# Kernel tuning notes

Hardware: AMD Instinct MI355X
Metric: run time of the kernel (lower is better)

The kernel has to match this reference:

```python
import jax, jax.numpy as jnp
import numpy as np

EPS = 1e-5  # BatchNorm eps (torch default)


def point_sample(feat, points):
    """Bilinear sample feat [B,C,Hf,Wf] at points [B,K,2] (x,y in [0,1]),
    matching F.grid_sample(2*p-1, mode='bilinear', padding_mode='zeros',
    align_corners=False)."""
    B, C, Hf, Wf = feat.shape
    x = points[..., 0] * Wf - 0.5  # [B,K] pixel coords
    y = points[..., 1] * Hf - 0.5
    x0f = jnp.floor(x); y0f = jnp.floor(y)
    wx = (x - x0f)[:, None, :]  # [B,1,K]
    wy = (y - y0f)[:, None, :]
    x0 = x0f.astype(jnp.int32); y0 = y0f.astype(jnp.int32)
    flat = feat.reshape(B, C, Hf * Wf)

    def gather(xi, yi):
        valid = ((xi >= 0) & (xi < Wf) & (yi >= 0) & (yi < Hf))[:, None, :]
        lin = jnp.clip(yi, 0, Hf - 1) * Wf + jnp.clip(xi, 0, Wf - 1)  # [B,K]
        idx = jnp.broadcast_to(lin[:, None, :], (B, C, lin.shape[1]))
        return jnp.take_along_axis(flat, idx, axis=2) * valid

    v00 = gather(x0, y0)
    v10 = gather(x0 + 1, y0)
    v01 = gather(x0, y0 + 1)
    v11 = gather(x0 + 1, y0 + 1)
    return (v00 * (1 - wx) * (1 - wy) + v10 * wx * (1 - wy)
            + v01 * (1 - wx) * wy + v11 * wx * wy)


def bn(x, g, b, m, v):
    # eval-mode BatchNorm1d over channel dim of [B,C,K]
    scale = (g / jnp.sqrt(v + EPS))[None, :, None]
    return (x - m[None, :, None]) * scale + b[None, :, None]


def setup_inputs() -> dict:
    key = jax.random.key(0)
    ks = jax.random.split(key, 20)
    B, H, W = 8, 512, 512
    Cf = 256
    d = {
        'uncertainty_map': jax.random.normal(ks[0], (B, 1, H, W), jnp.float32),
        'prev_mask': jax.random.uniform(ks[1], (B, 1, H, W), jnp.float32),
        'enc_f': jax.random.normal(ks[2], (B, Cf, 128, 128), jnp.float32),
        'w1': jax.random.normal(ks[3], (256, Cf + 1), jnp.float32) * 0.05,
        'b1': jax.random.normal(ks[4], (256,), jnp.float32) * 0.05,
        'g1': jnp.ones((256,), jnp.float32),
        'be1': jnp.zeros((256,), jnp.float32),
        'm1': jax.random.normal(ks[5], (256,), jnp.float32) * 0.1,
        'v1': jax.random.uniform(ks[6], (256,), jnp.float32) + 0.5,
        'w2': jax.random.normal(ks[7], (256, 256), jnp.float32) * 0.05,
        'b2': jax.random.normal(ks[8], (256,), jnp.float32) * 0.05,
        'g2': jnp.ones((256,), jnp.float32),
        'be2': jnp.zeros((256,), jnp.float32),
        'm2': jax.random.normal(ks[9], (256,), jnp.float32) * 0.1,
        'v2': jax.random.uniform(ks[10], (256,), jnp.float32) + 0.5,
        'w3': jax.random.normal(ks[11], (1, 256), jnp.float32) * 0.05,
        'b3': jax.random.normal(ks[12], (1,), jnp.float32) * 0.05,
    }
    return d


def reference(uncertainty_map, prev_mask, enc_f,
              w1, b1, g1, be1, m1, v1,
              w2, b2, g2, be2, m2, v2,
              w3, b3):
    B, C, H, W = prev_mask.shape
    K = H * W // 10
    # K least-uncertain points (topk largest=False)
    _, idx = jax.lax.top_k(-uncertainty_map.reshape(B, -1), K)  # [B,K] int32
    col = (idx % W).astype(jnp.float32)
    row = (idx // W).astype(jnp.float32)
    points = jnp.stack([(col + 0.5) / W, (row + 0.5) / H], axis=-1)  # [B,K,2]

    coarse = point_sample(prev_mask, points)  # [B,1,K]
    fine = point_sample(enc_f, points)        # [B,Cf,K]
    h = jnp.concatenate([coarse, fine], axis=1)  # [B,Cf+1,K]

    h = jax.nn.relu(bn(jnp.einsum('oc,bck->bok', w1, h) + b1[None, :, None], g1, be1, m1, v1))
    h = jax.nn.relu(bn(jnp.einsum('oc,bck->bok', w2, h) + b2[None, :, None], g2, be2, m2, v2))
    refined = jax.nn.sigmoid(jnp.einsum('oc,bck->bok', w3, h) + b3[None, :, None])  # [B,1,K]

    flat = prev_mask.reshape(B, C, H * W)
    bi = jnp.arange(B)[:, None, None]
    ci = jnp.arange(C)[None, :, None]
    out = flat.at[bi, ci, idx[:, None, :]].set(jnp.broadcast_to(refined, (B, C, K)))
    return out.reshape(B, C, H, W)
```

## Files before the change

### kernel.cpp

```cpp
#include <hip/hip_runtime.h>
#include <hip/hip_bf16.h>

#define HW_IMG 262144
#define KSEL   26214
#define NB     8
#define CF     256
#define LDACT  264
#define GBLK   410
#define MBLK   205
#define NPTS_PAD 26240

#define ACOL(c) ((c) ^ ((((c) >> 6) & 3) << 4))

typedef short    short8 __attribute__((ext_vector_type(8)));
typedef float    f32x4  __attribute__((ext_vector_type(4)));
typedef unsigned u32x2  __attribute__((ext_vector_type(2)));
typedef unsigned short u16x4 __attribute__((ext_vector_type(4)));

__device__ __forceinline__ unsigned f2key(float f){
    unsigned u = __builtin_bit_cast(unsigned, f);
    return (u & 0x80000000u) ? ~u : (u | 0x80000000u);
}
__device__ __forceinline__ unsigned short f2bf(float f){
    unsigned u = __builtin_bit_cast(unsigned, f);
    u = u + 0x7FFFu + ((u >> 16) & 1u);
    return (unsigned short)(u >> 16);
}
__device__ __forceinline__ float bf2f(unsigned short s){
    unsigned u = ((unsigned)s) << 16;
    return __builtin_bit_cast(float, u);
}

__global__ __launch_bounds__(256) void k_prep(
    const float* __restrict__ w1, const float* __restrict__ w2,
    const float* __restrict__ b1, const float* __restrict__ g1, const float* __restrict__ be1,
    const float* __restrict__ m1, const float* __restrict__ v1,
    const float* __restrict__ b2, const float* __restrict__ g2, const float* __restrict__ be2,
    const float* __restrict__ m2, const float* __restrict__ v2,
    unsigned short* __restrict__ w1p, unsigned short* __restrict__ w2p,
    float* __restrict__ c1, float* __restrict__ c2, float* __restrict__ w1c0)
{
    int tid = blockIdx.x * 256 + threadIdx.x;
    if (tid < 65536) {
        int o = tid >> 8, k = tid & 255;
        float scale = g1[o] * rsqrtf(v1[o] + 1e-5f);
        w1p[tid] = f2bf(w1[o * 257 + k + 1] * scale);
        if (k == 0) {
            c1[o] = (b1[o] - m1[o]) * scale + be1[o];
            w1c0[o] = w1[o * 257] * scale;
        }
    } else {
        int t2 = tid - 65536;
        int o = t2 >> 8;
        float scale = g2[o] * rsqrtf(v2[o] + 1e-5f);
        w2p[t2] = f2bf(w2[t2] * scale);
        if ((t2 & 255) == 0) c2[o] = (b2[o] - m2[o]) * scale + be2[o];
    }
}

__global__ __launch_bounds__(256) void k_transpose(
    const float* __restrict__ enc, unsigned short* __restrict__ encT)
{
    __shared__ __align__(16) unsigned short tile[64][72];
    int wg = blockIdx.x;
    int b = wg & 7;
    int r = wg >> 3;
    int pixbase = (r & 255) * 64;
    int chbase  = (r >> 8) * 64;
    int t = threadIdx.x;
    int pix = t & 63, cg = t >> 6;
    const float* src = enc + (size_t)b * CF * 16384;
#pragma unroll
    for (int i = 0; i < 16; i++) {
        int c = chbase + cg * 16 + i;
        float v = __builtin_nontemporal_load(&src[(size_t)c * 16384 + pixbase + pix]);
        tile[pix][cg * 16 + i] = f2bf(v);
    }
    __syncthreads();
    unsigned short* dst = encT + (size_t)b * 16384 * CF;
#pragma unroll
    for (int pass = 0; pass < 4; pass++) {
        int pl = pass * 16 + (t >> 4);
        int c4 = (t & 15) * 4;
        *(u16x4*)(dst + (size_t)(pixbase + pl) * CF + chbase + c4) = *(const u16x4*)&tile[pl][c4];
    }
}


__global__ __launch_bounds__(256) void k_histA(const float* __restrict__ unc, unsigned* __restrict__ hist)
{
    __shared__ unsigned lh[4][4096];
    int wg = blockIdx.x;
    int b = wg & 7, x = wg >> 3, t = threadIdx.x;
    int wv = t >> 6;
    for (int i = t; i < 4 * 4096; i += 256) ((unsigned*)lh)[i] = 0;
    __syncthreads();
    const float4* src = (const float4*)(unc + (size_t)b * HW_IMG + x * 4096);
    unsigned* mine = lh[wv];
#pragma unroll
    for (int j = 0; j < 4; j++) {
        float4 v = src[j * 256 + t];
        atomicAdd(&mine[f2key(v.x) >> 20], 1u);
        atomicAdd(&mine[f2key(v.y) >> 20], 1u);
        atomicAdd(&mine[f2key(v.z) >> 20], 1u);
        atomicAdd(&mine[f2key(v.w) >> 20], 1u);
    }
    __syncthreads();
    unsigned* gh = hist + (size_t)b * 4096;
    for (int i = t; i < 4096; i += 256) {
        unsigned c = lh[0][i] + lh[1][i] + lh[2][i] + lh[3][i];
        if (c) atomicAdd(&gh[i], c);
    }
}

__global__ __launch_bounds__(256) void k_histB(const float* __restrict__ unc,
    const unsigned* __restrict__ meta, unsigned* __restrict__ hist)
{
    __shared__ unsigned lh[4096];
    int wg = blockIdx.x;
    int b = wg & 7, x = wg >> 3, t = threadIdx.x;
// ... 102 lines not shown
__global__ __launch_bounds__(256) void k_emit(const float* __restrict__ unc,
    const unsigned* __restrict__ meta, const unsigned* __restrict__ offL,
    const unsigned* __restrict__ offE, unsigned* __restrict__ sel)
{
    int wg = blockIdx.x;
    int b = wg & 7, blk = wg >> 3, t = threadIdx.x;
    unsigned pivot = meta[b * 8 + 6], cless = meta[b * 8 + 5], r = KSEL - cless;
    int base = blk * 1024 + t * 4;
    const float4* src = (const float4*)(unc + (size_t)b * HW_IMG + blk * 1024);
    float4 v = src[t];
    unsigned key[4] = { f2key(v.x), f2key(v.y), f2key(v.z), f2key(v.w) };
    unsigned cl = 0, ce = 0;
#pragma unroll
    for (int j = 0; j < 4; j++) { cl += (key[j] < pivot); ce += (key[j] == pivot); }
    __shared__ unsigned sL[256], sE[256];
    sL[t] = cl; sE[t] = ce; __syncthreads();
    for (int off = 1; off < 256; off <<= 1) {
        unsigned aL = (t >= off) ? sL[t - off] : 0u;
        unsigned aE = (t >= off) ? sE[t - off] : 0u;
        __syncthreads();
        sL[t] += aL; sE[t] += aE;
        __syncthreads();
    }
    unsigned posL = offL[b * 256 + blk] + sL[t] - cl;
    unsigned posE = offE[b * 256 + blk] + sE[t] - ce;
    unsigned* sb = sel + (size_t)b * KSEL;
#pragma unroll
    for (int j = 0; j < 4; j++) {
        if (key[j] < pivot) { sb[posL++] = (unsigned)(base + j); }
        else if (key[j] == pivot) { if (posE < r) sb[cless + posE] = (unsigned)(base + j); posE++; }
    }
}

__global__ __launch_bounds__(256) void k_gather(
    const unsigned* __restrict__ sel, const unsigned short* __restrict__ encT,
    unsigned short* __restrict__ gout)
{
    int wg = blockIdx.x;
    int b  = wg & 7;
    int pbase = (wg >> 3) * 64;
    int t = threadIdx.x;
    const unsigned* selb = sel + (size_t)b * KSEL;

    int wv2 = t >> 6, l2 = t & 63;
    int g = l2 >> 2, sub = l2 & 3;
    int p = wv2 * 16 + g;
    int gi = pbase + p; if (gi >= KSEL) gi = KSEL - 1;
    unsigned id = selb[gi];
    int col = id & 511, row = (int)(id >> 9);
    float xf = (col - 1.5f) * 0.25f;
    float yf = (row - 1.5f) * 0.25f;
    float x0f = floorf(xf), y0f = floorf(yf);
    int x0 = (int)x0f, y0 = (int)y0f;
    float wx = xf - x0f, wy = yf - y0f;
    float wxa = (x0 >= 0) ? (1.f - wx) : 0.f;
    float wxb = (x0 <= 126) ? wx : 0.f;
    float wya = (y0 >= 0) ? (1.f - wy) : 0.f;
    float wyb = (y0 <= 126) ? wy : 0.f;
    int xc0 = x0 < 0 ? 0 : x0;
    int xc1 = (x0 + 1 > 127) ? 127 : x0 + 1;
    int yc0 = y0 < 0 ? 0 : y0;
    int yc1 = (y0 + 1 > 127) ? 127 : y0 + 1;
    float w00 = wxa * wya, w10 = wxb * wya, w01 = wxa * wyb, w11 = wxb * wyb;
    const unsigned short* bb = encT + (size_t)b * 16384 * CF;
    const unsigned short* p00 = bb + (size_t)(yc0 * 128 + xc0) * CF + sub * 8;
    const unsigned short* p10 = bb + (size_t)(yc0 * 128 + xc1) * CF + sub * 8;
    const unsigned short* p01 = bb + (size_t)(yc1 * 128 + xc0) * CF + sub * 8;
    const unsigned short* p11 = bb + (size_t)(yc1 * 128 + xc1) * CF + sub * 8;
    unsigned short* dst = gout + ((size_t)b * NPTS_PAD + pbase + p) * CF + sub * 8;
#pragma unroll 4
    for (int ch = 0; ch < 8; ch++) {
        int off = ch * 32;
        short8 va = *(const short8*)(p00 + off);
        short8 vb = *(const short8*)(p10 + off);
        short8 vc = *(const short8*)(p01 + off);
        short8 vd = *(const short8*)(p11 + off);
        short8 rr;
#pragma unroll
        for (int j = 0; j < 8; j++) {
            float f = w00 * bf2f((unsigned short)va[j]) + w10 * bf2f((unsigned short)vb[j])
                    + w01 * bf2f((unsigned short)vc[j]) + w11 * bf2f((unsigned short)vd[j]);
            rr[j] = (short)f2bf(f);
        }
        __builtin_nontemporal_store(rr, (short8*)(dst + off));
    }
}

__global__ __launch_bounds__(512, 4) void k_mlp(
    const unsigned* __restrict__ sel, const float* __restrict__ prev,
    const unsigned short* __restrict__ gout,
    const unsigned short* __restrict__ w1p, const unsigned short* __restrict__ w2p,
    const float* __restrict__ c1, const float* __restrict__ c2,
    const float* __restrict__ w3, const float* __restrict__ b3,
    const float* __restrict__ w1c0, float* __restrict__ out)
{
    __shared__ __align__(16) unsigned short act[128][LDACT];
    __shared__ float sPart[8][128];
    __shared__ float sCoarse[128];

    int wg = blockIdx.x;
    int b  = wg & 7;
    int pbase = (wg >> 3) * 128;
    int npts = KSEL - pbase; if (npts > 128) npts = 128;
    int t = threadIdx.x;
    const unsigned* selb = sel + (size_t)b * KSEL;

    const unsigned short* src = gout + ((size_t)b * NPTS_PAD + pbase) * CF;
#pragma unroll
    for (int i = 0; i < 8; i++) {
        int e = i * 4096 + t * 8;
        short8 v = __builtin_nontemporal_load((const short8*)(src + e));
        int pp = e >> 8, c = e & 255;
        *(short8*)&act[pp][ACOL(c)] = v;
    }
    if (t < 128) {
        int gi = pbase + t; if (gi >= KSEL) gi = KSEL - 1;
        unsigned id = selb[gi];
        sCoarse[t] = __builtin_nontemporal_load(&prev[(size_t)b * HW_IMG + id]);
    }
    __syncthreads();

    int w = t >> 6, l = t & 63;
    int lr = l & 15, lk = l >> 4;
    f32x4 acc[2][8];
#pragma unroll
    for (int m = 0; m < 2; m++)
#pragma unroll
        for (int n = 0; n < 8; n++) acc[m][n] = (f32x4){0.f, 0.f, 0.f, 0.f};

#pragma unroll
    for (int kk = 0; kk < 8; kk++) {
        int k0 = kk * 32 + lk * 8;
        int k0s = ACOL(k0);
        short8 afr[2], bfr[8];
#pragma unroll
        for (int m = 0; m < 2; m++)
            afr[m] = *(const short8*)(w1p + (size_t)(w * 32 + m * 16 + lr) * 256 + k0);
#pragma unroll
        for (int n = 0; n < 8; n++)
            bfr[n] = *(const short8*)&act[n * 16 + lr][k0s];
#pragma unroll
        for (int m = 0; m < 2; m++)
#pragma unroll
            for (int n = 0; n < 8; n++)
                acc[m][n] = __builtin_amdgcn_mfma_f32_16x16x32_bf16(afr[m], bfr[n], acc[m][n], 0, 0, 0);
    }
    __syncthreads();

#pragma unroll
    for (int m = 0; m < 2; m++) {
        int chb = w * 32 + m * 16 + lk * 4;
        int chbs = ACOL(chb);
        float c0 = c1[chb], cA = c1[chb + 1], cB = c1[chb + 2], cC = c1[chb + 3];
        float q0 = w1c0[chb], qA = w1c0[chb + 1], qB = w1c0[chb + 2], qC = w1c0[chb + 3];
#pragma unroll
        for (int n = 0; n < 8; n++) {
            int p = n * 16 + lr;
            float cv = sCoarse[p];
            float v0 = fmaxf(acc[m][n][0] + c0 + q0 * cv, 0.f);
            float v1 = fmaxf(acc[m][n][1] + cA + qA * cv, 0.f);
            float v2 = fmaxf(acc[m][n][2] + cB + qB * cv, 0.f);
            float v3 = fmaxf(acc[m][n][3] + cC + qC * cv, 0.f);
            u32x2 pk;
            pk[0] = (unsigned)f2bf(v0) | ((unsigned)f2bf(v1) << 16);
            pk[1] = (unsigned)f2bf(v2) | ((unsigned)f2bf(v3) << 16);
            *(u32x2*)&act[p][chbs] = pk;
        }
    }
    __syncthreads();

#pragma unroll
    for (int m = 0; m < 2; m++)
#pragma unroll
        for (int n = 0; n < 8; n++) acc[m][n] = (f32x4){0.f, 0.f, 0.f, 0.f};
#pragma unroll
    for (int kk = 0; kk < 8; kk++) {
        int k0 = kk * 32 + lk * 8;
        int k0s = ACOL(k0);
        short8 afr[2], bfr[8];
#pragma unroll
        for (int m = 0; m < 2; m++)
            afr[m] = *(const short8*)(w2p + (size_t)(w * 32 + m * 16 + lr) * 256 + k0);
#pragma unroll
        for (int n = 0; n < 8; n++)
            bfr[n] = *(const short8*)&act[n * 16 + lr][k0s];
#pragma unroll
        for (int m = 0; m < 2; m++)
#pragma unroll
            for (int n = 0; n < 8; n++)
                acc[m][n] = __builtin_amdgcn_mfma_f32_16x16x32_bf16(afr[m], bfr[n], acc[m][n], 0, 0, 0);
    }

    float part[8] = {0.f, 0.f, 0.f, 0.f, 0.f, 0.f, 0.f, 0.f};
#pragma unroll
    for (int m = 0; m < 2; m++) {
        int chb = w * 32 + m * 16 + lk * 4;
#pragma unroll
        for (int r = 0; r < 4; r++) {
            float wr = w3[chb + r];
            float cr = c2[chb + r];
#pragma unroll
            for (int n = 0; n < 8; n++)
                part[n] += wr * fmaxf(acc[m][n][r] + cr, 0.f);
        }
    }
#pragma unroll
    for (int n = 0; n < 8; n++) {
        part[n] += __shfl_xor(part[n], 16);
        part[n] += __shfl_xor(part[n], 32);
    }
    if (lk == 0) {
#pragma unroll
        for (int n = 0; n < 8; n++) sPart[w][n * 16 + lr] = part[n];
    }
    __syncthreads();
    if (t < 128 && t < npts) {
        float tot = b3[0];
#pragma unroll
        for (int ww = 0; ww < 8; ww++) tot += sPart[ww][t];
        float refined = 1.f / (1.f + __expf(-tot));
        unsigned id = selb[pbase + t];
        __builtin_nontemporal_store(refined, &out[(size_t)b * HW_IMG + id]);
    }
}

extern "C" void kernel_launch(void* const* d_in, const int* in_sizes, int n_in,
                              void* d_out, int out_size, void* d_ws, size_t ws_size,
                              hipStream_t stream)
{
    (void)in_sizes; (void)n_in; (void)out_size; (void)ws_size;
    const float* unc  = (const float*)d_in[0];
    const float* prev = (const float*)d_in[1];
    const float* enc  = (const float*)d_in[2];
    const float* w1   = (const float*)d_in[3];
    const float* b1   = (const float*)d_in[4];
    const float* g1   = (const float*)d_in[5];
    const float* be1  = (const float*)d_in[6];
    const float* m1   = (const float*)d_in[7];
    const float* v1   = (const float*)d_in[8];
    const float* w2   = (const float*)d_in[9];
    const float* b2   = (const float*)d_in[10];
    const float* g2   = (const float*)d_in[11];
    const float* be2  = (const float*)d_in[12];
    const float* m2   = (const float*)d_in[13];
    const float* v2   = (const float*)d_in[14];
    const float* w3   = (const float*)d_in[15];
    const float* b3   = (const float*)d_in[16];
    float* out = (float*)d_out;

    char* ws = (char*)d_ws;
    size_t off = 0;
    auto alloc = [&](size_t bytes) { size_t o = off; off += (bytes + 255) & ~(size_t)255; return o; };
    size_t o_encT = alloc((size_t)NB * 16384 * CF * 2);
    size_t o_gout = alloc((size_t)NB * NPTS_PAD * CF * 2);
    size_t o_w1p  = alloc((size_t)256 * 256 * 2);
    size_t o_w2p  = alloc((size_t)256 * 256 * 2);
    size_t o_c1   = alloc(256 * 4);
    size_t o_c2   = alloc(256 * 4);
    size_t o_w1c0 = alloc(256 * 4);
    size_t o_hist = alloc((size_t)3 * NB * 4096 * 4);
    size_t o_meta = alloc(NB * 8 * 4);
    size_t o_cntL = alloc(NB * 256 * 4);
    size_t o_cntE = alloc(NB * 256 * 4);
    size_t o_offL = alloc(NB * 256 * 4);
    size_t o_offE = alloc(NB * 256 * 4);
    size_t o_sel  = alloc((size_t)NB * KSEL * 4);

    unsigned short* encT = (unsigned short*)(ws + o_encT);
    unsigned short* goutp= (unsigned short*)(ws + o_gout);
    unsigned short* w1p  = (unsigned short*)(ws + o_w1p);
    unsigned short* w2p  = (unsigned short*)(ws + o_w2p);
    float* c1p = (float*)(ws + o_c1);
    float* c2p = (float*)(ws + o_c2);
    float* w1c0p = (float*)(ws + o_w1c0);
    unsigned* histA = (unsigned*)(ws + o_hist);
    unsigned* histB = histA + (size_t)NB * 4096;
    unsigned* histC = histB + (size_t)NB * 4096;
    unsigned* meta  = (unsigned*)(ws + o_meta);
    unsigned* cntL  = (unsigned*)(ws + o_cntL);
    unsigned* cntE  = (unsigned*)(ws + o_cntE);
    unsigned* offL  = (unsigned*)(ws + o_offL);
    unsigned* offE  = (unsigned*)(ws + o_offE);
    unsigned* sel   = (unsigned*)(ws + o_sel);

    hipMemsetAsync(ws + o_hist, 0, (size_t)3 * NB * 4096 * 4, stream);
    hipMemcpyAsync(d_out, (const void*)prev, (size_t)NB * HW_IMG * 4, hipMemcpyDeviceToDevice, stream);

    k_prep<<<512, 256, 0, stream>>>(w1, w2, b1, g1, be1, m1, v1, b2, g2, be2, m2, v2,
                                    w1p, w2p, c1p, c2p, w1c0p);
    k_transpose<<<8192, 256, 0, stream>>>(enc, encT);

    k_histA<<<512, 256, 0, stream>>>(unc, histA);
    k_find <<<NB, 256, 0, stream>>>(histA, meta, 16, 0);
    k_histB<<<512, 256, 0, stream>>>(unc, meta, histB);
    k_find <<<NB, 256, 0, stream>>>(histB, meta, 16, 1);
    k_histC<<<512, 256, 0, stream>>>(unc, meta, histC);
    k_find <<<NB, 256, 0, stream>>>(histC, meta, 1, 2);
    k_count<<<2048, 256, 0, stream>>>(unc, meta, cntL, cntE);
    k_scan <<<NB, 64, 0, stream>>>(cntL, cntE, offL, offE);
    k_emit <<<2048, 256, 0, stream>>>(unc, meta, offL, offE, sel);

    k_gather<<<GBLK * NB, 256, 0, stream>>>(sel, encT, goutp);
    k_mlp   <<<MBLK * NB, 512, 0, stream>>>(sel, prev, goutp, w1p, w2p,
                                            c1p, c2p, w3, b3, w1c0p, out);
}
```

Measured before the change: 218.6 us.

## Fuse bilinear gather into MLP kernel with two-half software pipeline

```diff
diff --git a/kernel.cpp b/kernel.cpp
--- a/kernel.cpp
+++ b/kernel.cpp
@@ -6,9 +6,7 @@
 #define NB     8
 #define CF     256
 #define LDACT  264
-#define GBLK   410
 #define MBLK   205
-#define NPTS_PAD 26240
 
 #define ACOL(c) ((c) ^ ((((c) >> 6) & 3) << 4))
 
@@ -254,189 +252,177 @@
     }
 }
 
-__global__ __launch_bounds__(256) void k_gather(
-    const unsigned* __restrict__ sel, const unsigned short* __restrict__ encT,
-    unsigned short* __restrict__ gout)
-{
-    int wg = blockIdx.x;
-    int b  = wg & 7;
-    int pbase = (wg >> 3) * 64;
-    int t = threadIdx.x;
-    const unsigned* selb = sel + (size_t)b * KSEL;
-
-    int wv2 = t >> 6, l2 = t & 63;
-    int g = l2 >> 2, sub = l2 & 3;
-    int p = wv2 * 16 + g;
-    int gi = pbase + p; if (gi >= KSEL) gi = KSEL - 1;
-    unsigned id = selb[gi];
-    int col = id & 511, row = (int)(id >> 9);
-    float xf = (col - 1.5f) * 0.25f;
-    float yf = (row - 1.5f) * 0.25f;
-    float x0f = floorf(xf), y0f = floorf(yf);
-    int x0 = (int)x0f, y0 = (int)y0f;
-    float wx = xf - x0f, wy = yf - y0f;
-    float wxa = (x0 >= 0) ? (1.f - wx) : 0.f;
-    float wxb = (x0 <= 126) ? wx : 0.f;
-    float wya = (y0 >= 0) ? (1.f - wy) : 0.f;
-    float wyb = (y0 <= 126) ? wy : 0.f;
-    int xc0 = x0 < 0 ? 0 : x0;
-    int xc1 = (x0 + 1 > 127) ? 127 : x0 + 1;
-    int yc0 = y0 < 0 ? 0 : y0;
-    int yc1 = (y0 + 1 > 127) ? 127 : y0 + 1;
-    float w00 = wxa * wya, w10 = wxb * wya, w01 = wxa * wyb, w11 = wxb * wyb;
-    const unsigned short* bb = encT + (size_t)b * 16384 * CF;
-    const unsigned short* p00 = bb + (size_t)(yc0 * 128 + xc0) * CF + sub * 8;
-    const unsigned short* p10 = bb + (size_t)(yc0 * 128 + xc1) * CF + sub * 8;
-    const unsigned short* p01 = bb + (size_t)(yc1 * 128 + xc0) * CF + sub * 8;
-    const unsigned short* p11 = bb + (size_t)(yc1 * 128 + xc1) * CF + sub * 8;
-    unsigned short* dst = gout + ((size_t)b * NPTS_PAD + pbase + p) * CF + sub * 8;
-#pragma unroll 4
-    for (int ch = 0; ch < 8; ch++) {
-        int off = ch * 32;
-        short8 va = *(const short8*)(p00 + off);
-        short8 vb = *(const short8*)(p10 + off);
-        short8 vc = *(const short8*)(p01 + off);
-        short8 vd = *(const short8*)(p11 + off);
-        short8 rr;
-#pragma unroll
-        for (int j = 0; j < 8; j++) {
-            float f = w00 * bf2f((unsigned short)va[j]) + w10 * bf2f((unsigned short)vb[j])
-                    + w01 * bf2f((unsigned short)vc[j]) + w11 * bf2f((unsigned short)vd[j]);
-            rr[j] = (short)f2bf(f);
-        }
-        __builtin_nontemporal_store(rr, (short8*)(dst + off));
-    }
-}
-
 __global__ __launch_bounds__(512, 4) void k_mlp(
     const unsigned* __restrict__ sel, const float* __restrict__ prev,
-    const unsigned short* __restrict__ gout,
+    const unsigned short* __restrict__ encT,
     const unsigned short* __restrict__ w1p, const unsigned short* __restrict__ w2p,
     const float* __restrict__ c1, const float* __restrict__ c2,
     const float* __restrict__ w3, const float* __restrict__ b3,
     const float* __restrict__ w1c0, float* __restrict__ out)
 {
-    __shared__ __align__(16) unsigned short act[128][LDACT];
+    __shared__ __align__(16) unsigned short act[2][64][LDACT];
     __shared__ float sPart[8][128];
     __shared__ float sCoarse[128];
 
     int wg = blockIdx.x;
     int b  = wg & 7;
     int pbase = (wg >> 3) * 128;
-    int npts = KSEL - pbase; if (npts > 128) npts = 128;
     int t = threadIdx.x;
     const unsigned* selb = sel + (size_t)b * KSEL;
-
-    const unsigned short* src = gout + ((size_t)b * NPTS_PAD + pbase) * CF;
-#pragma unroll
-    for (int i = 0; i < 8; i++) {
-        int e = i * 4096 + t * 8;
-        short8 v = __builtin_nontemporal_load((const short8*)(src + e));
-        int pp = e >> 8, c = e & 255;
-        *(short8*)&act[pp][ACOL(c)] = v;
-    }
+    const unsigned short* eb = encT + (size_t)b * 16384 * CF;
+
+    auto GATHER = [&](int h) {
+        int p  = t >> 3;
+        int s  = t & 7;
+        int gi = pbase + h * 64 + p; if (gi >= KSEL) gi = KSEL - 1;
+        unsigned id = selb[gi];
+        int col = id & 511, row = (int)(id >> 9);
+        float xf = (col - 1.5f) * 0.25f;
+        float yf = (row - 1.5f) * 0.25f;
+        float x0f = floorf(xf), y0f = floorf(yf);
+        int x0 = (int)x0f, y0 = (int)y0f;
+        float wx = xf - x0f, wy = yf - y0f;
+        float wxa = (x0 >= 0) ? (1.f - wx) : 0.f;
+        float wxb = (x0 <= 126) ? wx : 0.f;
+        float wya = (y0 >= 0) ? (1.f - wy) : 0.f;
+        float wyb = (y0 <= 126) ? wy : 0.f;
+        int xc0 = x0 < 0 ? 0 : x0;
+        int xc1 = (x0 + 1 > 127) ? 127 : x0 + 1;
+        int yc0 = y0 < 0 ? 0 : y0;
+        int yc1 = (y0 + 1 > 127) ? 127 : y0 + 1;
+        float w00 = wxa * wya, w10 = wxb * wya, w01 = wxa * wyb, w11 = wxb * wyb;
+        const unsigned short* p00 = eb + (size_t)(yc0 * 128 + xc0) * CF + s * 32;
+        const unsigned short* p10 = eb + (size_t)(yc0 * 128 + xc1) * CF + s * 32;
+        const unsigned short* p01 = eb + (size_t)(yc1 * 128 + xc0) * CF + s * 32;
+        const unsigned short* p11 = eb + (size_t)(yc1 * 128 + xc1) * CF + s * 32;
+#pragma unroll 2
+        for (int j = 0; j < 4; j++) {
+            int off = j * 8;
+            short8 va = *(const short8*)(p00 + off);
+            short8 vb = *(const short8*)(p10 + off);
+            short8 vc = *(const short8*)(p01 + off);
+            short8 vd = *(const short8*)(p11 + off);
+            short8 rr;
+#pragma unroll
+            for (int q = 0; q < 8; q++) {
+                float f = w00 * bf2f((unsigned short)va[q]) + w10 * bf2f((unsigned short)vb[q])
+                        + w01 * bf2f((unsigned short)vc[q]) + w11 * bf2f((unsigned short)vd[q]);
+                rr[q] = (short)f2bf(f);
+            }
+            int c = s * 32 + off;
+            *(short8*)&act[h][p][ACOL(c)] = rr;
+        }
+    };
+
+    GATHER(0);
     if (t < 128) {
         int gi = pbase + t; if (gi >= KSEL) gi = KSEL - 1;
-        unsigned id = selb[gi];
-        sCoarse[t] = __builtin_nontemporal_load(&prev[(size_t)b * HW_IMG + id]);
+        sCoarse[t] = prev[(size_t)b * HW_IMG + selb[gi]];
     }
     __syncthreads();
 
     int w = t >> 6, l = t & 63;
     int lr = l & 15, lk = l >> 4;
-    f32x4 acc[2][8];
-#pragma unroll
-    for (int m = 0; m < 2; m++)
-#pragma unroll
-        for (int n = 0; n < 8; n++) acc[m][n] = (f32x4){0.f, 0.f, 0.f, 0.f};
-
-#pragma unroll
-    for (int kk = 0; kk < 8; kk++) {
-        int k0 = kk * 32 + lk * 8;
-        int k0s = ACOL(k0);
-        short8 afr[2], bfr[8];
+
+#pragma unroll
+    for (int h = 0; h < 2; h++) {
+        f32x4 acc[2][4];
 #pragma unroll
         for (int m = 0; m < 2; m++)
-            afr[m] = *(const short8*)(w1p + (size_t)(w * 32 + m * 16 + lr) * 256 + k0);
-#pragma unroll
-        for (int n = 0; n < 8; n++)
-            bfr[n] = *(const short8*)&act[n * 16 + lr][k0s];
+#pragma unroll
+            for (int n = 0; n < 4; n++) acc[m][n] = (f32x4){0.f, 0.f, 0.f, 0.f};
+
+#pragma unroll
+        for (int kk = 0; kk < 8; kk++) {
+            int k0 = kk * 32 + lk * 8;
+            int k0s = ACOL(k0);
+            short8 afr[2], bfr[4];
+#pragma unroll
+            for (int m = 0; m < 2; m++)
+                afr[m] = *(const short8*)(w1p + (size_t)(w * 32 + m * 16 + lr) * 256 + k0);
+#pragma unroll
+            for (int n = 0; n < 4; n++)
+                bfr[n] = *(const short8*)&act[h][n * 16 + lr][k0s];
+#pragma unroll
+            for (int m = 0; m < 2; m++)
+#pragma unroll
+                for (int n = 0; n < 4; n++)
+                    acc[m][n] = __builtin_amdgcn_mfma_f32_16x16x32_bf16(afr[m], bfr[n], acc[m][n], 0, 0, 0);
+        }
+        if (h == 0) GATHER(1);
+        __syncthreads();
+
+#pragma unroll
+        for (int m = 0; m < 2; m++) {
+            int chb = w * 32 + m * 16 + lk * 4;
+            int chbs = ACOL(chb);
+            float c0 = c1[chb], cA = c1[chb + 1], cB = c1[chb + 2], cC = c1[chb + 3];
+            float q0 = w1c0[chb], qA = w1c0[chb + 1], qB = w1c0[chb + 2], qC = w1c0[chb + 3];
+#pragma unroll
+            for (int n = 0; n < 4; n++) {
+                int p = n * 16 + lr;
+                float cv = sCoarse[h * 64 + p];
+                float v0 = fmaxf(acc[m][n][0] + c0 + q0 * cv, 0.f);
+                float v1 = fmaxf(acc[m][n][1] + cA + qA * cv, 0.f);
+                float v2 = fmaxf(acc[m][n][2] + cB + qB * cv, 0.f);
+                float v3 = fmaxf(acc[m][n][3] + cC + qC * cv, 0.f);
+                u32x2 pk;
+                pk[0] = (unsigned)f2bf(v0) | ((unsigned)f2bf(v1) << 16);
+                pk[1] = (unsigned)f2bf(v2) | ((unsigned)f2bf(v3) << 16);
+                *(u32x2*)&act[h][p][chbs] = pk;
+            }
+        }
+        __syncthreads();
+
 #pragma unroll
         for (int m = 0; m < 2; m++)
 #pragma unroll
-            for (int n = 0; n < 8; n++)
-                acc[m][n] = __builtin_amdgcn_mfma_f32_16x16x32_bf16(afr[m], bfr[n], acc[m][n], 0, 0, 0);
-    }
-    __syncthreads();
-
-#pragma unroll
-    for (int m = 0; m < 2; m++) {
-        int chb = w * 32 + m * 16 + lk * 4;
-        int chbs = ACOL(chb);
-        float c0 = c1[chb], cA = c1[chb + 1], cB = c1[chb + 2], cC = c1[chb + 3];
-        float q0 = w1c0[chb], qA = w1c0[chb + 1], qB = w1c0[chb + 2], qC = w1c0[chb + 3];
-#pragma unroll
-        for (int n = 0; n < 8; n++) {
-            int p = n * 16 + lr;
-            float cv = sCoarse[p];
-            float v0 = fmaxf(acc[m][n][0] + c0 + q0 * cv, 0.f);
-            float v1 = fmaxf(acc[m][n][1] + cA + qA * cv, 0.f);
-            float v2 = fmaxf(acc[m][n][2] + cB + qB * cv, 0.f);
-            float v3 = fmaxf(acc[m][n][3] + cC + qC * cv, 0.f);
-            u32x2 pk;
-            pk[0] = (unsigned)f2bf(v0) | ((unsigned)f2bf(v1) << 16);
-            pk[1] = (unsigned)f2bf(v2) | ((unsigned)f2bf(v3) << 16);
-            *(u32x2*)&act[p][chbs] = pk;
-        }
-    }
-    __syncthreads();
-
-#pragma unroll
-    for (int m = 0; m < 2; m++)
-#pragma unroll
-        for (int n = 0; n < 8; n++) acc[m][n] = (f32x4){0.f, 0.f, 0.f, 0.f};
-#pragma unroll
-    for (int kk = 0; kk < 8; kk++) {
-        int k0 = kk * 32 + lk * 8;
-        int k0s = ACOL(k0);
-        short8 afr[2], bfr[8];
-#pragma unroll
-        for (int m = 0; m < 2; m++)
-            afr[m] = *(const short8*)(w2p + (size_t)(w * 32 + m * 16 + lr) * 256 + k0);
-#pragma unroll
-        for (int n = 0; n < 8; n++)
-            bfr[n] = *(const short8*)&act[n * 16 + lr][k0s];
-#pragma unroll
-        for (int m = 0; m < 2; m++)
-#pragma unroll
-            for (int n = 0; n < 8; n++)
-                acc[m][n] = __builtin_amdgcn_mfma_f32_16x16x32_bf16(afr[m], bfr[n], acc[m][n], 0, 0, 0);
-    }
-
-    float part[8] = {0.f, 0.f, 0.f, 0.f, 0.f, 0.f, 0.f, 0.f};
-#pragma unroll
-    for (int m = 0; m < 2; m++) {
-        int chb = w * 32 + m * 16 + lk * 4;
-#pragma unroll
-        for (int r = 0; r < 4; r++) {
-            float wr = w3[chb + r];
-            float cr = c2[chb + r];
-#pragma unroll
-            for (int n = 0; n < 8; n++)
-                part[n] += wr * fmaxf(acc[m][n][r] + cr, 0.f);
-        }
-    }
-#pragma unroll
-    for (int n = 0; n < 8; n++) {
-        part[n] += __shfl_xor(part[n], 16);
-        part[n] += __shfl_xor(part[n], 32);
-    }
-    if (lk == 0) {
-#pragma unroll
-        for (int n = 0; n < 8; n++) sPart[w][n * 16 + lr] = part[n];
-    }
-    __syncthreads();
-    if (t < 128 && t < npts) {
+            for (int n = 0; n < 4; n++) acc[m][n] = (f32x4){0.f, 0.f, 0.f, 0.f};
+#pragma unroll
+        for (int kk = 0; kk < 8; kk++) {
+            int k0 = kk * 32 + lk * 8;
+            int k0s = ACOL(k0);
+            short8 afr[2], bfr[4];
+#pragma unroll
+            for (int m = 0; m < 2; m++)
+                afr[m] = *(const short8*)(w2p + (size_t)(w * 32 + m * 16 + lr) * 256 + k0);
+#pragma unroll
+            for (int n = 0; n < 4; n++)
+                bfr[n] = *(const short8*)&act[h][n * 16 + lr][k0s];
+#pragma unroll
+            for (int m = 0; m < 2; m++)
+#pragma unroll
+                for (int n = 0; n < 4; n++)
+                    acc[m][n] = __builtin_amdgcn_mfma_f32_16x16x32_bf16(afr[m], bfr[n], acc[m][n], 0, 0, 0);
+        }
+
+        float part[4] = {0.f, 0.f, 0.f, 0.f};
+#pragma unroll
+        for (int m = 0; m < 2; m++) {
+            int chb = w * 32 + m * 16 + lk * 4;
+#pragma unroll
+            for (int r = 0; r < 4; r++) {
+                float wr = w3[chb + r];
+                float cr = c2[chb + r];
+#pragma unroll
+                for (int n = 0; n < 4; n++)
+                    part[n] += wr * fmaxf(acc[m][n][r] + cr, 0.f);
+            }
+        }
+#pragma unroll
+        for (int n = 0; n < 4; n++) {
+            part[n] += __shfl_xor(part[n], 16);
+            part[n] += __shfl_xor(part[n], 32);
+        }
+        if (lk == 0) {
+#pragma unroll
+            for (int n = 0; n < 4; n++) sPart[w][h * 64 + n * 16 + lr] = part[n];
+        }
+    }
+    __syncthreads();
+
+    int npts = KSEL - pbase; if (npts > 128) npts = 128;
+    if (t < npts) {
         float tot = b3[0];
 #pragma unroll
         for (int ww = 0; ww < 8; ww++) tot += sPart[ww][t];
@@ -474,7 +460,6 @@
     size_t off = 0;
     auto alloc = [&](size_t bytes) { size_t o = off; off += (bytes + 255) & ~(size_t)255; return o; };
     size_t o_encT = alloc((size_t)NB * 16384 * CF * 2);
-    size_t o_gout = alloc((size_t)NB * NPTS_PAD * CF * 2);
     size_t o_w1p  = alloc((size_t)256 * 256 * 2);
     size_t o_w2p  = alloc((size_t)256 * 256 * 2);
     size_t o_c1   = alloc(256 * 4);
@@ -489,7 +474,6 @@
     size_t o_sel  = alloc((size_t)NB * KSEL * 4);
 
     unsigned short* encT = (unsigned short*)(ws + o_encT);
-    unsigned short* goutp= (unsigned short*)(ws + o_gout);
     unsigned short* w1p  = (unsigned short*)(ws + o_w1p);
     unsigned short* w2p  = (unsigned short*)(ws + o_w2p);
     float* c1p = (float*)(ws + o_c1);
@@ -522,7 +506,6 @@
     k_scan <<<NB, 64, 0, stream>>>(cntL, cntE, offL, offE);
     k_emit <<<2048, 256, 0, stream>>>(unc, meta, offL, offE, sel);
 
-    k_gather<<<GBLK * NB, 256, 0, stream>>>(sel, encT, goutp);
-    k_mlp   <<<MBLK * NB, 512, 0, stream>>>(sel, prev, goutp, w1p, w2p,
-                                            c1p, c2p, w3, b3, w1c0p, out);
-}
+    k_mlp<<<MBLK * NB, 512, 0, stream>>>(sel, prev, encT, w1p, w2p,
+                                         c1p, c2p, w3, b3, w1c0p, out);
+}
```

Measured after the change: 246.6 us. 1.13x slower.

## Make MLP kernel persistent with register-resident weights and double-buffered LDS staging

Applied to the files above, without the earlier changes.

```diff
diff --git a/kernel.cpp b/kernel.cpp
--- a/kernel.cpp
+++ b/kernel.cpp
@@ -5,12 +5,9 @@
 #define KSEL   26214
 #define NB     8
 #define CF     256
-#define LDACT  264
 #define GBLK   410
 #define MBLK   205
 #define NPTS_PAD 26240
-
-#define ACOL(c) ((c) ^ ((((c) >> 6) & 3) << 4))
 
 typedef short    short8 __attribute__((ext_vector_type(8)));
 typedef float    f32x4  __attribute__((ext_vector_type(4)));
@@ -29,6 +26,11 @@
 __device__ __forceinline__ float bf2f(unsigned short s){
     unsigned u = ((unsigned)s) << 16;
     return __builtin_bit_cast(float, u);
+}
+__device__ __forceinline__ void gload_lds16(const void* g, void* l){
+    __builtin_amdgcn_global_load_lds(
+        (const __attribute__((address_space(1))) unsigned*)g,
+        (__attribute__((address_space(3))) unsigned*)l, 16, 0, 0);
 }
 
 __global__ __launch_bounds__(256) void k_prep(
@@ -85,7 +87,6 @@
         *(u16x4*)(dst + (size_t)(pixbase + pl) * CF + chbase + c4) = *(const u16x4*)&tile[pl][c4];
     }
 }
-
 
 __global__ __launch_bounds__(256) void k_histA(const float* __restrict__ unc, unsigned* __restrict__ hist)
 {
@@ -289,7 +290,8 @@
     const unsigned short* p10 = bb + (size_t)(yc0 * 128 + xc1) * CF + sub * 8;
     const unsigned short* p01 = bb + (size_t)(yc1 * 128 + xc0) * CF + sub * 8;
     const unsigned short* p11 = bb + (size_t)(yc1 * 128 + xc1) * CF + sub * 8;
-    unsigned short* dst = gout + ((size_t)b * NPTS_PAD + pbase + p) * CF + sub * 8;
+    unsigned short* dstrow = gout + ((size_t)b * NPTS_PAD + pbase + p) * CF;
+    int key = (p & 7) << 3;
 #pragma unroll 4
     for (int ch = 0; ch < 8; ch++) {
         int off = ch * 32;
@@ -304,11 +306,12 @@
                     + w01 * bf2f((unsigned short)vc[j]) + w11 * bf2f((unsigned short)vd[j]);
             rr[j] = (short)f2bf(f);
         }
-        __builtin_nontemporal_store(rr, (short8*)(dst + off));
-    }
-}
-
-__global__ __launch_bounds__(512, 4) void k_mlp(
+        int dstoff = (sub * 8 + off) ^ key;
+        __builtin_nontemporal_store(rr, (short8*)(dstrow + dstoff));
+    }
+}
+
+__global__ __launch_bounds__(512, 2) void k_mlp(
     const unsigned* __restrict__ sel, const float* __restrict__ prev,
     const unsigned short* __restrict__ gout,
     const unsigned short* __restrict__ w1p, const unsigned short* __restrict__ w2p,
@@ -316,133 +319,153 @@
     const float* __restrict__ w3, const float* __restrict__ b3,
     const float* __restrict__ w1c0, float* __restrict__ out)
 {
-    __shared__ __align__(16) unsigned short act[128][LDACT];
+    __shared__ __align__(16) unsigned short act[2][128][256];
     __shared__ float sPart[8][128];
-    __shared__ float sCoarse[128];
+    __shared__ float sCoarse[2][128];
+    __shared__ float c1s[256], qs[256], c2s[256], w3s[256];
 
     int wg = blockIdx.x;
     int b  = wg & 7;
-    int pbase = (wg >> 3) * 128;
-    int npts = KSEL - pbase; if (npts > 128) npts = 128;
+    int slot = wg >> 3;
     int t = threadIdx.x;
-    const unsigned* selb = sel + (size_t)b * KSEL;
-
-    const unsigned short* src = gout + ((size_t)b * NPTS_PAD + pbase) * CF;
-#pragma unroll
-    for (int i = 0; i < 8; i++) {
-        int e = i * 4096 + t * 8;
-        short8 v = __builtin_nontemporal_load((const short8*)(src + e));
-        int pp = e >> 8, c = e & 255;
-        *(short8*)&act[pp][ACOL(c)] = v;
-    }
-    if (t < 128) {
-        int gi = pbase + t; if (gi >= KSEL) gi = KSEL - 1;
-        unsigned id = selb[gi];
-        sCoarse[t] = __builtin_nontemporal_load(&prev[(size_t)b * HW_IMG + id]);
-    }
-    __syncthreads();
-
     int w = t >> 6, l = t & 63;
     int lr = l & 15, lk = l >> 4;
-    f32x4 acc[2][8];
+    const unsigned* selb = sel + (size_t)b * KSEL;
+    const float* prevb = prev + (size_t)b * HW_IMG;
+    const unsigned short* gb = gout + (size_t)b * NPTS_PAD * CF;
+
+    short8 w1f[2][8], w2f[2][8];
 #pragma unroll
     for (int m = 0; m < 2; m++)
 #pragma unroll
-        for (int n = 0; n < 8; n++) acc[m][n] = (f32x4){0.f, 0.f, 0.f, 0.f};
-
-#pragma unroll
-    for (int kk = 0; kk < 8; kk++) {
-        int k0 = kk * 32 + lk * 8;
-        int k0s = ACOL(k0);
-        short8 afr[2], bfr[8];
+        for (int kk = 0; kk < 8; kk++) {
+            size_t r = (size_t)(w * 32 + m * 16 + lr) * 256 + kk * 32 + lk * 8;
+            w1f[m][kk] = *(const short8*)(w1p + r);
+            w2f[m][kk] = *(const short8*)(w2p + r);
+        }
+    if (t < 256) { c1s[t] = c1[t]; qs[t] = w1c0[t]; }
+    else { int u = t - 256; c2s[u] = c2[u]; w3s[u] = w3[u]; }
+    float b3v = b3[0];
+
+    auto STAGE = [&](int bb, int tile) {
+        const char* g = (const char*)(gb + (size_t)tile * 128 * CF) + w * 8192 + l * 16;
+        char* lp = (char*)&act[bb][w * 16][0];
+#pragma unroll
+        for (int i = 0; i < 8; i++)
+            gload_lds16(g + i * 1024, lp + i * 1024);
+    };
+    auto COARSE = [&](int bb, int tile) {
+        if (t < 128) {
+            int gi = tile * 128 + t; if (gi >= KSEL) gi = KSEL - 1;
+            sCoarse[bb][t] = prevb[selb[gi]];
+        }
+    };
+
+    int cur = 0;
+    STAGE(0, slot);
+    COARSE(0, slot);
+    __syncthreads();
+
+    for (int tile = slot; tile < MBLK; tile += 32) {
+        int nxt = tile + 32;
+        if (nxt < MBLK) { STAGE(cur ^ 1, nxt); COARSE(cur ^ 1, nxt); }
+
+        int colx = (lr & 7) << 3;
+
+        f32x4 acc[2][8];
 #pragma unroll
         for (int m = 0; m < 2; m++)
-            afr[m] = *(const short8*)(w1p + (size_t)(w * 32 + m * 16 + lr) * 256 + k0);
-#pragma unroll
-        for (int n = 0; n < 8; n++)
-            bfr[n] = *(const short8*)&act[n * 16 + lr][k0s];
+#pragma unroll
+            for (int n = 0; n < 8; n++) acc[m][n] = (f32x4){0.f, 0.f, 0.f, 0.f};
+#pragma unroll
+        for (int kk = 0; kk < 8; kk++) {
+            int cb = (kk * 32 + lk * 8) ^ colx;
+            short8 bfr[8];
+#pragma unroll
+            for (int n = 0; n < 8; n++)
+                bfr[n] = *(const short8*)&act[cur][n * 16 + lr][cb];
+#pragma unroll
+            for (int m = 0; m < 2; m++)
+#pragma unroll
+                for (int n = 0; n < 8; n++)
+                    acc[m][n] = __builtin_amdgcn_mfma_f32_16x16x32_bf16(w1f[m][kk], bfr[n], acc[m][n], 0, 0, 0);
+        }
+        __syncthreads();
+
+#pragma unroll
+        for (int m = 0; m < 2; m++) {
+            int chb = w * 32 + m * 16 + lk * 4;
+            float c0 = c1s[chb], cA = c1s[chb + 1], cB = c1s[chb + 2], cC = c1s[chb + 3];
+            float q0 = qs[chb],  qA = qs[chb + 1],  qB = qs[chb + 2],  qC = qs[chb + 3];
+#pragma unroll
+            for (int n = 0; n < 8; n++) {
+                int p = n * 16 + lr;
+                float cv = sCoarse[cur][p];
+                float v0 = fmaxf(acc[m][n][0] + c0 + q0 * cv, 0.f);
+                float v1 = fmaxf(acc[m][n][1] + cA + qA * cv, 0.f);
+                float v2 = fmaxf(acc[m][n][2] + cB + qB * cv, 0.f);
+                float v3 = fmaxf(acc[m][n][3] + cC + qC * cv, 0.f);
+                u32x2 pk;
+                pk[0] = (unsigned)f2bf(v0) | ((unsigned)f2bf(v1) << 16);
+                pk[1] = (unsigned)f2bf(v2) | ((unsigned)f2bf(v3) << 16);
+                *(u32x2*)&act[cur][p][chb ^ ((p & 7) << 3)] = pk;
+            }
+        }
+        __syncthreads();
+
 #pragma unroll
         for (int m = 0; m < 2; m++)
 #pragma unroll
+            for (int n = 0; n < 8; n++) acc[m][n] = (f32x4){0.f, 0.f, 0.f, 0.f};
+#pragma unroll
+        for (int kk = 0; kk < 8; kk++) {
+            int cb = (kk * 32 + lk * 8) ^ colx;
+            short8 bfr[8];
+#pragma unroll
             for (int n = 0; n < 8; n++)
-                acc[m][n] = __builtin_amdgcn_mfma_f32_16x16x32_bf16(afr[m], bfr[n], acc[m][n], 0, 0, 0);
-    }
-    __syncthreads();
-
-#pragma unroll
-    for (int m = 0; m < 2; m++) {
-        int chb = w * 32 + m * 16 + lk * 4;
-        int chbs = ACOL(chb);
-        float c0 = c1[chb], cA = c1[chb + 1], cB = c1[chb + 2], cC = c1[chb + 3];
-        float q0 = w1c0[chb], qA = w1c0[chb + 1], qB = w1c0[chb + 2], qC = w1c0[chb + 3];
+                bfr[n] = *(const short8*)&act[cur][n * 16 + lr][cb];
+#pragma unroll
+            for (int m = 0; m < 2; m++)
+#pragma unroll
+                for (int n = 0; n < 8; n++)
+                    acc[m][n] = __builtin_amdgcn_mfma_f32_16x16x32_bf16(w2f[m][kk], bfr[n], acc[m][n], 0, 0, 0);
+        }
+
+        float part[8] = {0.f, 0.f, 0.f, 0.f, 0.f, 0.f, 0.f, 0.f};
+#pragma unroll
+        for (int m = 0; m < 2; m++) {
+            int chb = w * 32 + m * 16 + lk * 4;
+#pragma unroll
+            for (int r = 0; r < 4; r++) {
+                float wr = w3s[chb + r];
+                float cr = c2s[chb + r];
+#pragma unroll
+                for (int n = 0; n < 8; n++)
+                    part[n] += wr * fmaxf(acc[m][n][r] + cr, 0.f);
+            }
+        }
 #pragma unroll
         for (int n = 0; n < 8; n++) {
-            int p = n * 16 + lr;
-            float cv = sCoarse[p];
-            float v0 = fmaxf(acc[m][n][0] + c0 + q0 * cv, 0.f);
-            float v1 = fmaxf(acc[m][n][1] + cA + qA * cv, 0.f);
-            float v2 = fmaxf(acc[m][n][2] + cB + qB * cv, 0.f);
-            float v3 = fmaxf(acc[m][n][3] + cC + qC * cv, 0.f);
-            u32x2 pk;
-            pk[0] = (unsigned)f2bf(v0) | ((unsigned)f2bf(v1) << 16);
-            pk[1] = (unsigned)f2bf(v2) | ((unsigned)f2bf(v3) << 16);
-            *(u32x2*)&act[p][chbs] = pk;
-        }
-    }
-    __syncthreads();
-
-#pragma unroll
-    for (int m = 0; m < 2; m++)
-#pragma unroll
-        for (int n = 0; n < 8; n++) acc[m][n] = (f32x4){0.f, 0.f, 0.f, 0.f};
-#pragma unroll
-    for (int kk = 0; kk < 8; kk++) {
-        int k0 = kk * 32 + lk * 8;
-        int k0s = ACOL(k0);
-        short8 afr[2], bfr[8];
-#pragma unroll
-        for (int m = 0; m < 2; m++)
-            afr[m] = *(const short8*)(w2p + (size_t)(w * 32 + m * 16 + lr) * 256 + k0);
-#pragma unroll
-        for (int n = 0; n < 8; n++)
-            bfr[n] = *(const short8*)&act[n * 16 + lr][k0s];
-#pragma unroll
-        for (int m = 0; m < 2; m++)
-#pragma unroll
-            for (int n = 0; n < 8; n++)
-                acc[m][n] = __builtin_amdgcn_mfma_f32_16x16x32_bf16(afr[m], bfr[n], acc[m][n], 0, 0, 0);
-    }
-
-    float part[8] = {0.f, 0.f, 0.f, 0.f, 0.f, 0.f, 0.f, 0.f};
-#pragma unroll
-    for (int m = 0; m < 2; m++) {
-        int chb = w * 32 + m * 16 + lk * 4;
-#pragma unroll
-        for (int r = 0; r < 4; r++) {
-            float wr = w3[chb + r];
-            float cr = c2[chb + r];
-#pragma unroll
-            for (int n = 0; n < 8; n++)
-                part[n] += wr * fmaxf(acc[m][n][r] + cr, 0.f);
-        }
-    }
-#pragma unroll
-    for (int n = 0; n < 8; n++) {
-        part[n] += __shfl_xor(part[n], 16);
-        part[n] += __shfl_xor(part[n], 32);
-    }
-    if (lk == 0) {
-#pragma unroll
-        for (int n = 0; n < 8; n++) sPart[w][n * 16 + lr] = part[n];
-    }
-    __syncthreads();
-    if (t < 128 && t < npts) {
-        float tot = b3[0];
-#pragma unroll
-        for (int ww = 0; ww < 8; ww++) tot += sPart[ww][t];
-        float refined = 1.f / (1.f + __expf(-tot));
-        unsigned id = selb[pbase + t];
-        __builtin_nontemporal_store(refined, &out[(size_t)b * HW_IMG + id]);
+            part[n] += __shfl_xor(part[n], 16);
+            part[n] += __shfl_xor(part[n], 32);
+        }
+        if (lk == 0) {
+#pragma unroll
+            for (int n = 0; n < 8; n++) sPart[w][n * 16 + lr] = part[n];
+        }
+        __syncthreads();
+
+        if (t < 128) {
+            int gi = tile * 128 + t;
+            if (gi < KSEL) {
+                float tot = b3v;
+#pragma unroll
+                for (int ww = 0; ww < 8; ww++) tot += sPart[ww][t];
+                float refined = 1.f / (1.f + __expf(-tot));
+                __builtin_nontemporal_store(refined, &out[(size_t)b * HW_IMG + selb[gi]]);
+            }
+        }
+        cur ^= 1;
     }
 }
 
@@ -523,6 +546,6 @@
     k_emit <<<2048, 256, 0, stream>>>(unc, meta, offL, offE, sel);
 
     k_gather<<<GBLK * NB, 256, 0, stream>>>(sel, encT, goutp);
-    k_mlp   <<<MBLK * NB, 512, 0, stream>>>(sel, prev, goutp, w1p, w2p,
-                                            c1p, c2p, w3, b3, w1c0p, out);
-}
+    k_mlp   <<<256, 512, 0, stream>>>(sel, prev, goutp, w1p, w2p,
+                                      c1p, c2p, w3, b3, w1c0p, out);
+}
```

After: 220.2 us. Within noise of the previous version (+0.7%).

## Apply first linear layer before bilinear sampling and fuse it into the transpose

Applied to the files above, without the earlier changes.

```diff
diff --git a/kernel.cpp b/kernel.cpp
--- a/kernel.cpp
+++ b/kernel.cpp
@@ -58,34 +58,87 @@
     }
 }
 
-__global__ __launch_bounds__(256) void k_transpose(
-    const float* __restrict__ enc, unsigned short* __restrict__ encT)
-{
+__global__ __launch_bounds__(256, 3) void k_e1(
+    const float* __restrict__ enc, const unsigned short* __restrict__ w1p,
+    unsigned short* __restrict__ e1)
+{
+    __shared__ __align__(16) unsigned short actT[64][LDACT];
     __shared__ __align__(16) unsigned short tile[64][72];
     int wg = blockIdx.x;
     int b = wg & 7;
-    int r = wg >> 3;
-    int pixbase = (r & 255) * 64;
-    int chbase  = (r >> 8) * 64;
+    int pixbase = (wg >> 3) * 64;
     int t = threadIdx.x;
+    const float* src = enc + (size_t)b * CF * 16384;
+
     int pix = t & 63, cg = t >> 6;
-    const float* src = enc + (size_t)b * CF * 16384;
-#pragma unroll
-    for (int i = 0; i < 16; i++) {
-        int c = chbase + cg * 16 + i;
-        float v = __builtin_nontemporal_load(&src[(size_t)c * 16384 + pixbase + pix]);
-        tile[pix][cg * 16 + i] = f2bf(v);
-    }
-    __syncthreads();
-    unsigned short* dst = encT + (size_t)b * 16384 * CF;
-#pragma unroll
-    for (int pass = 0; pass < 4; pass++) {
-        int pl = pass * 16 + (t >> 4);
-        int c4 = (t & 15) * 4;
-        *(u16x4*)(dst + (size_t)(pixbase + pl) * CF + chbase + c4) = *(const u16x4*)&tile[pl][c4];
-    }
-}
-
+#pragma unroll
+    for (int cc = 0; cc < 4; cc++) {
+#pragma unroll
+        for (int i = 0; i < 16; i++) {
+            int c = cc * 64 + cg * 16 + i;
+            float v = __builtin_nontemporal_load(&src[(size_t)c * 16384 + pixbase + pix]);
+            tile[pix][cg * 16 + i] = f2bf(v);
+        }
+        __syncthreads();
+#pragma unroll
+        for (int pass = 0; pass < 4; pass++) {
+            int pl = pass * 16 + (t >> 4);
+            int c4 = (t & 15) * 4;
+            *(u16x4*)&actT[pl][ACOL(cc * 64 + c4)] = *(const u16x4*)&tile[pl][c4];
+        }
+        __syncthreads();
+    }
+
+    int w = t >> 6, l = t & 63;
+    int lr = l & 15, lk = l >> 4;
+    f32x4 acc[4][4];
+#pragma unroll
+    for (int m = 0; m < 4; m++)
+#pragma unroll
+        for (int n = 0; n < 4; n++) acc[m][n] = (f32x4){0.f, 0.f, 0.f, 0.f};
+#pragma unroll
+    for (int kk = 0; kk < 8; kk++) {
+        int k0 = kk * 32 + lk * 8;
+        int k0s = ACOL(k0);
+        short8 afr[4], bfr[4];
+#pragma unroll
+        for (int m = 0; m < 4; m++)
+            afr[m] = *(const short8*)(w1p + (size_t)(w * 64 + m * 16 + lr) * 256 + k0);
+#pragma unroll
+        for (int n = 0; n < 4; n++)
+            bfr[n] = *(const short8*)&actT[n * 16 + lr][k0s];
+#pragma unroll
+        for (int m = 0; m < 4; m++)
+#pragma unroll
+            for (int n = 0; n < 4; n++)
+                acc[m][n] = __builtin_amdgcn_mfma_f32_16x16x32_bf16(afr[m], bfr[n], acc[m][n], 0, 0, 0);
+    }
+    __syncthreads();
+
+#pragma unroll
+    for (int m = 0; m < 4; m++) {
+        int chb = w * 64 + m * 16 + lk * 4;
+        int chbs = ACOL(chb);
+#pragma unroll
+        for (int n = 0; n < 4; n++) {
+            int p = n * 16 + lr;
+            u32x2 pk;
+            pk[0] = (unsigned)f2bf(acc[m][n][0]) | ((unsigned)f2bf(acc[m][n][1]) << 16);
+            pk[1] = (unsigned)f2bf(acc[m][n][2]) | ((unsigned)f2bf(acc[m][n][3]) << 16);
+            *(u32x2*)&actT[p][chbs] = pk;
+        }
+    }
+    __syncthreads();
+
+    unsigned short* dst = e1 + ((size_t)b * 16384 + pixbase) * CF;
+#pragma unroll
+    for (int i = 0; i < 8; i++) {
+        int e = i * 2048 + t * 8;
+        int pp = e >> 8, c = e & 255;
+        short8 v = *(const short8*)&actT[pp][ACOL(c)];
+        __builtin_nontemporal_store(v, (short8*)(dst + e));
+    }
+}
 
 __global__ __launch_bounds__(256) void k_histA(const float* __restrict__ unc, unsigned* __restrict__ hist)
 {
@@ -255,8 +308,9 @@
 }
 
 __global__ __launch_bounds__(256) void k_gather(
-    const unsigned* __restrict__ sel, const unsigned short* __restrict__ encT,
-    unsigned short* __restrict__ gout)
+    const unsigned* __restrict__ sel, const unsigned short* __restrict__ e1,
+    const float* __restrict__ prev, const float* __restrict__ c1,
+    const float* __restrict__ w1c0, unsigned short* __restrict__ gout)
 {
     int wg = blockIdx.x;
     int b  = wg & 7;
@@ -269,6 +323,7 @@
     int p = wv2 * 16 + g;
     int gi = pbase + p; if (gi >= KSEL) gi = KSEL - 1;
     unsigned id = selb[gi];
+    float cv = prev[(size_t)b * HW_IMG + id];
     int col = id & 511, row = (int)(id >> 9);
     float xf = (col - 1.5f) * 0.25f;
     float yf = (row - 1.5f) * 0.25f;
@@ -284,7 +339,7 @@
     int yc0 = y0 < 0 ? 0 : y0;
     int yc1 = (y0 + 1 > 127) ? 127 : y0 + 1;
     float w00 = wxa * wya, w10 = wxb * wya, w01 = wxa * wyb, w11 = wxb * wyb;
-    const unsigned short* bb = encT + (size_t)b * 16384 * CF;
+    const unsigned short* bb = e1 + (size_t)b * 16384 * CF;
     const unsigned short* p00 = bb + (size_t)(yc0 * 128 + xc0) * CF + sub * 8;
     const unsigned short* p10 = bb + (size_t)(yc0 * 128 + xc1) * CF + sub * 8;
     const unsigned short* p01 = bb + (size_t)(yc1 * 128 + xc0) * CF + sub * 8;
@@ -293,6 +348,11 @@
 #pragma unroll 4
     for (int ch = 0; ch < 8; ch++) {
         int off = ch * 32;
+        int chb = sub * 8 + off;
+        float4 ca = *(const float4*)(c1 + chb);
+        float4 cb = *(const float4*)(c1 + chb + 4);
+        float4 qa = *(const float4*)(w1c0 + chb);
+        float4 qb = *(const float4*)(w1c0 + chb + 4);
         short8 va = *(const short8*)(p00 + off);
         short8 vb = *(const short8*)(p10 + off);
         short8 vc = *(const short8*)(p01 + off);
@@ -302,23 +362,21 @@
         for (int j = 0; j < 8; j++) {
             float f = w00 * bf2f((unsigned short)va[j]) + w10 * bf2f((unsigned short)vb[j])
                     + w01 * bf2f((unsigned short)vc[j]) + w11 * bf2f((unsigned short)vd[j]);
-            rr[j] = (short)f2bf(f);
+            float bias = (j < 4 ? ca[j] : cb[j - 4]) + (j < 4 ? qa[j] : qb[j - 4]) * cv;
+            rr[j] = (short)f2bf(fmaxf(f + bias, 0.f));
         }
         __builtin_nontemporal_store(rr, (short8*)(dst + off));
     }
 }
 
 __global__ __launch_bounds__(512, 4) void k_mlp(
-    const unsigned* __restrict__ sel, const float* __restrict__ prev,
-    const unsigned short* __restrict__ gout,
-    const unsigned short* __restrict__ w1p, const unsigned short* __restrict__ w2p,
-    const float* __restrict__ c1, const float* __restrict__ c2,
+    const unsigned* __restrict__ sel, const unsigned short* __restrict__ gout,
+    const unsigned short* __restrict__ w2p, const float* __restrict__ c2,
     const float* __restrict__ w3, const float* __restrict__ b3,
-    const float* __restrict__ w1c0, float* __restrict__ out)
+    float* __restrict__ out)
 {
     __shared__ __align__(16) unsigned short act[128][LDACT];
     __shared__ float sPart[8][128];
-    __shared__ float sCoarse[128];
 
     int wg = blockIdx.x;
     int b  = wg & 7;
@@ -335,11 +393,6 @@
         int pp = e >> 8, c = e & 255;
         *(short8*)&act[pp][ACOL(c)] = v;
     }
-    if (t < 128) {
-        int gi = pbase + t; if (gi >= KSEL) gi = KSEL - 1;
-        unsigned id = selb[gi];
-        sCoarse[t] = __builtin_nontemporal_load(&prev[(size_t)b * HW_IMG + id]);
-    }
     __syncthreads();
 
     int w = t >> 6, l = t & 63;
@@ -350,51 +403,6 @@
 #pragma unroll
         for (int n = 0; n < 8; n++) acc[m][n] = (f32x4){0.f, 0.f, 0.f, 0.f};
 
-#pragma unroll
-    for (int kk = 0; kk < 8; kk++) {
-        int k0 = kk * 32 + lk * 8;
-        int k0s = ACOL(k0);
-        short8 afr[2], bfr[8];
-#pragma unroll
-        for (int m = 0; m < 2; m++)
-            afr[m] = *(const short8*)(w1p + (size_t)(w * 32 + m * 16 + lr) * 256 + k0);
-#pragma unroll
-        for (int n = 0; n < 8; n++)
-            bfr[n] = *(const short8*)&act[n * 16 + lr][k0s];
-#pragma unroll
-        for (int m = 0; m < 2; m++)
-#pragma unroll
-            for (int n = 0; n < 8; n++)
-                acc[m][n] = __builtin_amdgcn_mfma_f32_16x16x32_bf16(afr[m], bfr[n], acc[m][n], 0, 0, 0);
-    }
-    __syncthreads();
-
-#pragma unroll
-    for (int m = 0; m < 2; m++) {
-        int chb = w * 32 + m * 16 + lk * 4;
-        int chbs = ACOL(chb);
-        float c0 = c1[chb], cA = c1[chb + 1], cB = c1[chb + 2], cC = c1[chb + 3];
-        float q0 = w1c0[chb], qA = w1c0[chb + 1], qB = w1c0[chb + 2], qC = w1c0[chb + 3];
-#pragma unroll
-        for (int n = 0; n < 8; n++) {
-            int p = n * 16 + lr;
-            float cv = sCoarse[p];
-            float v0 = fmaxf(acc[m][n][0] + c0 + q0 * cv, 0.f);
-            float v1 = fmaxf(acc[m][n][1] + cA + qA * cv, 0.f);
-            float v2 = fmaxf(acc[m][n][2] + cB + qB * cv, 0.f);
-            float v3 = fmaxf(acc[m][n][3] + cC + qC * cv, 0.f);
-            u32x2 pk;
-            pk[0] = (unsigned)f2bf(v0) | ((unsigned)f2bf(v1) << 16);
-            pk[1] = (unsigned)f2bf(v2) | ((unsigned)f2bf(v3) << 16);
-            *(u32x2*)&act[p][chbs] = pk;
-        }
-    }
-    __syncthreads();
-
-#pragma unroll
-    for (int m = 0; m < 2; m++)
-#pragma unroll
-        for (int n = 0; n < 8; n++) acc[m][n] = (f32x4){0.f, 0.f, 0.f, 0.f};
 #pragma unroll
     for (int kk = 0; kk < 8; kk++) {
         int k0 = kk * 32 + lk * 8;
@@ -473,7 +481,7 @@
     char* ws = (char*)d_ws;
     size_t off = 0;
     auto alloc = [&](size_t bytes) { size_t o = off; off += (bytes + 255) & ~(size_t)255; return o; };
-    size_t o_encT = alloc((size_t)NB * 16384 * CF * 2);
+    size_t o_e1   = alloc((size_t)NB * 16384 * CF * 2);
     size_t o_gout = alloc((size_t)NB * NPTS_PAD * CF * 2);
     size_t o_w1p  = alloc((size_t)256 * 256 * 2);
     size_t o_w2p  = alloc((size_t)256 * 256 * 2);
@@ -488,7 +496,7 @@
     size_t o_offE = alloc(NB * 256 * 4);
     size_t o_sel  = alloc((size_t)NB * KSEL * 4);
 
-    unsigned short* encT = (unsigned short*)(ws + o_encT);
+    unsigned short* e1p  = (unsigned short*)(ws + o_e1);
     unsigned short* goutp= (unsigned short*)(ws + o_gout);
     unsigned short* w1p  = (unsigned short*)(ws + o_w1p);
     unsigned short* w2p  = (unsigned short*)(ws + o_w2p);
@@ -510,7 +518,7 @@
 
     k_prep<<<512, 256, 0, stream>>>(w1, w2, b1, g1, be1, m1, v1, b2, g2, be2, m2, v2,
                                     w1p, w2p, c1p, c2p, w1c0p);
-    k_transpose<<<8192, 256, 0, stream>>>(enc, encT);
+    k_e1  <<<2048, 256, 0, stream>>>(enc, w1p, e1p);
 
     k_histA<<<512, 256, 0, stream>>>(unc, histA);
     k_find <<<NB, 256, 0, stream>>>(histA, meta, 16, 0);
@@ -522,7 +530,6 @@
     k_scan <<<NB, 64, 0, stream>>>(cntL, cntE, offL, offE);
     k_emit <<<2048, 256, 0, stream>>>(unc, meta, offL, offE, sel);
 
-    k_gather<<<GBLK * NB, 256, 0, stream>>>(sel, encT, goutp);
-    k_mlp   <<<MBLK * NB, 512, 0, stream>>>(sel, prev, goutp, w1p, w2p,
-                                            c1p, c2p, w3, b3, w1c0p, out);
-}
+    k_gather<<<GBLK * NB, 256, 0, stream>>>(sel, e1p, prev, c1p, w1c0p, goutp);
+    k_mlp   <<<MBLK * NB, 512, 0, stream>>>(sel, goutp, w2p, c2p, w3, b3, out);
+}
```

Result: slower. 271.9 us (+24.4%).
